# Performance work log

Hardware: AMD Instinct MI355X
Metric: run time of the kernel (lower is better)

The kernel has to match this reference:

```python
import jax, jax.numpy as jnp
import numpy as np

B, C, W, H = 8, 256, 64, 64
C8 = C // 8


def setup_inputs() -> dict:
    key = jax.random.key(0)
    ks = jax.random.split(key, 8)
    # xavier_uniform for 1x1 convs: bound = sqrt(6/(fan_in+fan_out))
    def xavier(k, out_c, in_c):
        bound = np.sqrt(6.0 / (in_c + out_c))
        return jax.random.uniform(k, (out_c, in_c), jnp.float32, -bound, bound)
    return {
        "x": jax.random.normal(ks[0], (B, C, W, H), jnp.float32),
        "Wf": xavier(ks[1], C8, C),
        "bf": jnp.zeros((C8,), jnp.float32),
        "Wg": xavier(ks[2], C8, C),
        "bg": jnp.zeros((C8,), jnp.float32),
        "Wh": xavier(ks[3], C, C),
        "bh": jnp.zeros((C,), jnp.float32),
        "gamma": jnp.zeros((1,), jnp.float32),
    }


def reference(x, Wf, bf, Wg, bg, Wh, bh, gamma):
    b, c, w, h = x.shape
    n = w * h
    xf = x.reshape(b, c, n)                                   # (B, C, N)
    # 1x1 convs == per-position channel GEMMs
    f = jnp.einsum('oc,bcn->bon', Wf, xf) + bf[None, :, None]  # (B, C/8, N)
    g = jnp.einsum('oc,bcn->bon', Wg, xf) + bg[None, :, None]  # (B, C/8, N)
    hh = jnp.einsum('oc,bcn->bon', Wh, xf) + bh[None, :, None] # (B, C, N)
    # attention[b,i,j] = softmax_j( f[b,:,i] . g[b,:,j] )
    att = jax.nn.softmax(jnp.einsum('boi,boj->bij', f, g), axis=-1)
    # torch.bmm(h, attention): out[b,c,i] = sum_k h[b,c,k] * att[b,k,i]
    sa = jnp.einsum('bck,bki->bci', hh, att).reshape(b, c, w, h)
    return gamma * sa + x
```

## Files before the change

kernel.cpp:

```cpp
#include <hip/hip_runtime.h>
#include <hip/hip_bf16.h>

#define BB 8
#define CC 256
#define NN 4096
#define LOG2E 1.44269504088896340736f
#define SHIFT 48.0f

typedef __attribute__((ext_vector_type(8))) short short8;
typedef __attribute__((ext_vector_type(4))) float f32x4;

static __device__ __forceinline__ unsigned short f2b(float x) {
  __hip_bfloat16 h = __float2bfloat16(x);
  return *reinterpret_cast<unsigned short*>(&h);
}
static __device__ __forceinline__ unsigned int pk2(float a, float b) {
  return (unsigned int)f2b(a) | ((unsigned int)f2b(b) << 16);
}


__global__ __launch_bounds__(256) void k_wprep(
    const float* __restrict__ Wf, const float* __restrict__ bfv,
    const float* __restrict__ Wg, const float* __restrict__ bgv,
    const float* __restrict__ Wh, const float* __restrict__ bhv,
    unsigned short* __restrict__ wA, float* __restrict__ ball)
{
  const int t = threadIdx.x;
  const int fi = blockIdx.x * 4 + (t >> 6);
  const int l = t & 63;
  const int mg = fi >> 3, kg = fi & 7;
  const int o = mg * 16 + (l & 15);
  const int c0 = kg * 32 + (l >> 4) * 8;
  const float* src; float scale = 1.0f;
  if (o < 32)      { src = Wf + (size_t)o * CC; scale = LOG2E; }
  else if (o < 64) { src = Wg + (size_t)(o - 32) * CC; }
  else             { src = Wh + (size_t)(o - 64) * CC; }
  float4 a = *(const float4*)(src + c0);
  float4 c = *(const float4*)(src + c0 + 4);
  short8 v;
  v[0] = (short)f2b(a.x * scale); v[1] = (short)f2b(a.y * scale);
  v[2] = (short)f2b(a.z * scale); v[3] = (short)f2b(a.w * scale);
  v[4] = (short)f2b(c.x * scale); v[5] = (short)f2b(c.y * scale);
  v[6] = (short)f2b(c.z * scale); v[7] = (short)f2b(c.w * scale);
  *(short8*)(wA + (size_t)fi * 512 + l * 8) = v;
  if (blockIdx.x == 0 && t < 320)
    ball[t] = (t < 32) ? bfv[t] * LOG2E : (t < 64) ? bgv[t - 32] : bhv[t - 64];
}

__global__ __launch_bounds__(512) void k_fgh(
    const float* __restrict__ x, const unsigned short* __restrict__ wA,
    const float* __restrict__ ball,
    unsigned short* __restrict__ fA, unsigned short* __restrict__ gB,
    unsigned short* __restrict__ hA)
{
  __shared__ __align__(16) char smem[41984];
  unsigned short* xb = (unsigned short*)smem;
  unsigned short* TL = (unsigned short*)smem;
  const int bid = blockIdx.x;
  const int b = bid & 7, i0 = (bid >> 3) * 64;
  const int t = threadIdx.x, w = t >> 6, l = t & 63;
  const int ig_w = w & 3, mg0 = (w >> 2) * 10;
  f32x4 acc[10] = {};
  for (int cc = 0; cc < 4; ++cc) {
    __syncthreads();
    {
      short8 v;
      const float* xp = x + ((size_t)b * CC + cc * 64 + w * 8) * NN + i0 + l;
      #pragma unroll
      for (int e = 0; e < 8; ++e) v[e] = (short)f2b(xp[(size_t)e * NN]);
      int frag = (w >> 2) * 4 + (l >> 4);
      int lp = (w & 3) * 16 + (l & 15);
      *(short8*)(xb + (frag * 64 + lp) * 8) = v;
    }
    __syncthreads();
    #pragma unroll
    for (int kg2 = 0; kg2 < 2; ++kg2) {
      short8 bfrag = *(const short8*)(xb + ((kg2 * 4 + ig_w) * 64 + l) * 8);
      int kg = cc * 2 + kg2;
      #pragma unroll
      for (int j = 0; j < 10; ++j) {
        short8 afrag = *(const short8*)(wA +
            ((size_t)((mg0 + j) * 8 + kg)) * 512 + l * 8);
        acc[j] = __builtin_amdgcn_mfma_f32_16x16x32_bf16(afrag, bfrag, acc[j], 0, 0, 0);
      }
    }
  }
  __syncthreads();
  #pragma unroll
  for (int j = 0; j < 10; ++j) {
    int ob = (mg0 + j) * 16 + (l >> 4) * 4;
    float4 bl = *(const float4*)(ball + ob);
    int irow = ig_w * 16 + (l & 15);
    ushort4 pv;
    pv.x = f2b(acc[j][0] + bl.x); pv.y = f2b(acc[j][1] + bl.y);
    pv.z = f2b(acc[j][2] + bl.z); pv.w = f2b(acc[j][3] + bl.w);
    *(ushort4*)(TL + irow * 328 + ob) = pv;
  }
  __syncthreads();
  if (t < 256) {
    int kg_p = t >> 6;
    int o8 = (l >> 4) * 8;
    int irow = kg_p * 16 + (l & 15);
    short8 vf = *(const short8*)(TL + irow * 328 + o8);
    short8 vg = *(const short8*)(TL + irow * 328 + 32 + o8);
    size_t kgG = (size_t)b * 256 + (i0 >> 4) + kg_p;
    *(short8*)(fA + kgG * 512 + l * 8) = vf;
    *(short8*)(gB + kgG * 512 + l * 8) = vg;
  }
  #pragma unroll
  for (int q = 0; q < 4; ++q) {
    int slot = t + q * 512;
    int fr = slot >> 6, ll = slot & 63;
    int cg = fr >> 1, kcl = fr & 1;
    int orow = 64 + cg * 16 + (ll & 15);
    int pbase = kcl * 32 + (ll >> 4) * 8;
    short8 v;
    #pragma unroll
    for (int e = 0; e < 8; ++e) v[e] = (short)TL[(pbase + e) * 328 + orow];
    size_t idx = (((size_t)b * 16 + cg) * 128 + (i0 >> 5) + kcl) * 512 + ll * 8;
    *(short8*)(hA + idx) = v;
  }
}

__global__ __launch_bounds__(512) void k_stats(
    const unsigned short* __restrict__ fA, const unsigned short* __restrict__ gB,
    float* __restrict__ cshift)
{
  __shared__ __align__(16) unsigned short sg[2][16 * 512];
  const int bid = blockIdx.x;
  const int b = bid & 7, kt = bid >> 3;
  const int t = threadIdx.x, w = t >> 6, l = t & 63;
  const int li = l & 15, lh = l >> 4;
  short8 af = *(const short8*)(fA + ((size_t)b * 256 + kt * 8 + w) * 512 + l * 8);
  const unsigned short* gb = gB + (size_t)b * 256 * 512;
  f32x4 zero = {0.f, 0.f, 0.f, 0.f};
  {
    uint4 v0 = *(const uint4*)(gb + ((size_t)(w * 2 + 0) * 64 + l) * 8);
    uint4 v1 = *(const uint4*)(gb + ((size_t)(w * 2 + 1) * 64 + l) * 8);
    *(uint4*)(&sg[0][((w * 2 + 0) * 64 + l) * 8]) = v0;
    *(uint4*)(&sg[0][((w * 2 + 1) * 64 + l) * 8]) = v1;
  }
  __syncthreads();
  float s[4] = {0.f, 0.f, 0.f, 0.f};
  for (int jt = 0; jt < 16; ++jt) {
    if (jt < 15) {
      uint4 v0 = *(const uint4*)(gb + ((size_t)((jt + 1) * 16 + w * 2 + 0) * 64 + l) * 8);
      uint4 v1 = *(const uint4*)(gb + ((size_t)((jt + 1) * 16 + w * 2 + 1) * 64 + l) * 8);
      unsigned short* dst = &sg[(jt + 1) & 1][0];
      *(uint4*)(dst + ((w * 2 + 0) * 64 + l) * 8) = v0;
      *(uint4*)(dst + ((w * 2 + 1) * 64 + l) * 8) = v1;
    }
    const unsigned short* src = &sg[jt & 1][0];
    #pragma unroll
    for (int jf = 0; jf < 16; ++jf) {
      short8 bfrag = *(const short8*)(src + (jf * 64 + l) * 8);
      f32x4 d = __builtin_amdgcn_mfma_f32_16x16x32_bf16(af, bfrag, zero, 0, 0, 0);
      s[0] += exp2f(d[0] - SHIFT);
      s[1] += exp2f(d[1] - SHIFT);
      s[2] += exp2f(d[2] - SHIFT);
      s[3] += exp2f(d[3] - SHIFT);
    }
    __syncthreads();
  }
  #pragma unroll
  for (int mk = 1; mk < 16; mk <<= 1)
    #pragma unroll
    for (int r = 0; r < 4; ++r) s[r] += __shfl_xor(s[r], mk);
  if (li == 0) {
    #pragma unroll
    for (int r = 0; r < 4; ++r) {
      size_t idx = (size_t)b * NN + (kt * 8 + w) * 16 + lh * 4 + r;
      cshift[idx] = SHIFT + log2f(fmaxf(s[r], 1e-30f));
    }
  }
}

__global__ __launch_bounds__(512, 4) void k_out(
    const unsigned short* __restrict__ fA, const unsigned short* __restrict__ gB,
    const unsigned short* __restrict__ hA,
    const float* __restrict__ csv,
    const float* __restrict__ x, const float* __restrict__ gamma,
    float* __restrict__ out)
{
  __shared__ __align__(16) unsigned short pbuf[2 * 16 * 512];
  const int bid = blockIdx.x;
  const int b = bid & 7, i0 = (bid >> 3) * 64;
  const int t = threadIdx.x, w = t >> 6, l = t & 63;
  const int li = l & 15, lh = l >> 4;
  const unsigned short* fAb = fA + ((size_t)b * 256 + w) * 512 + l * 8;
  const unsigned short* hAb = hA + ((size_t)b * 16 + w * 2) * (size_t)128 * 512 + l * 8;
  const float* cs = csv + (size_t)b * NN + w * 16 + lh * 4;
  short8 g[4];
  #pragma unroll
  for (int ig = 0; ig < 4; ++ig)
    g[ig] = *(const short8*)(gB + ((size_t)b * 256 + (i0 >> 4) + ig) * 512 + l * 8);
  const int pl = ((w & 1) * 2 + (lh >> 1)) * 16 + li;
  const int pwo = pl * 8 + (lh & 1) * 4;
  f32x4 zero = {0.f, 0.f, 0.f, 0.f};
  f32x4 acc[2][4] = {};
  short8 afc = *(const short8*)(fAb);
  float4 ccc = *(const float4*)(cs);
  #pragma unroll
  for (int ig = 0; ig < 4; ++ig) {
    f32x4 sfr = __builtin_amdgcn_mfma_f32_16x16x32_bf16(afc, g[ig], zero, 0, 0, 0);
    uint2 v;
    v.x = pk2(exp2f(sfr[0] - ccc.x), exp2f(sfr[1] - ccc.y));
    v.y = pk2(exp2f(sfr[2] - ccc.z), exp2f(sfr[3] - ccc.w));
    *(uint2*)(pbuf + ((size_t)((w >> 1) * 4 + ig)) * 512 + pwo) = v;
  }
  afc = *(const short8*)(fAb + (size_t)8 * 512);
  ccc = *(const float4*)(cs + 128);
  __syncthreads();
  for (int ch = 0; ch < 32; ++ch) {
    unsigned short* pb  = pbuf + (ch & 1) * (16 * 512);
    unsigned short* pnx = pbuf + ((ch + 1) & 1) * (16 * 512);
    short8 hf[8];
    #pragma unroll
    for (int cg = 0; cg < 2; ++cg)
      #pragma unroll
      for (int kb = 0; kb < 4; ++kb)
        hf[cg * 4 + kb] = *(const short8*)(hAb +
            ((size_t)cg * 128 + ch * 4 + kb) * 512);
    if (ch < 31) {
      #pragma unroll
      for (int ig = 0; ig < 4; ++ig) {
        f32x4 sfr = __builtin_amdgcn_mfma_f32_16x16x32_bf16(afc, g[ig], zero, 0, 0, 0);
        uint2 v;
        v.x = pk2(exp2f(sfr[0] - ccc.x), exp2f(sfr[1] - ccc.y));
        v.y = pk2(exp2f(sfr[2] - ccc.z), exp2f(sfr[3] - ccc.w));
        *(uint2*)(pnx + ((size_t)((w >> 1) * 4 + ig)) * 512 + pwo) = v;
      }
      const int ch2 = (ch < 30) ? (ch + 2) : 31;
      afc = *(const short8*)(fAb + (size_t)ch2 * 8 * 512);
      ccc = *(const float4*)(cs + ch2 * 128);
    }
    __builtin_amdgcn_s_setprio(1);
    #pragma unroll
    for (int kb = 0; kb < 4; ++kb)
      #pragma unroll
      for (int ig = 0; ig < 4; ++ig) {
        short8 pf = *(const short8*)(pb + ((kb * 4 + ig) * 64 + l) * 8);
        acc[0][ig] = __builtin_amdgcn_mfma_f32_16x16x32_bf16(pf, hf[kb], acc[0][ig], 0, 0, 0);
        acc[1][ig] = __builtin_amdgcn_mfma_f32_16x16x32_bf16(pf, hf[4 + kb], acc[1][ig], 0, 0, 0);
      }
    __builtin_amdgcn_s_setprio(0);
    __syncthreads();
  }
  const float gm = gamma[0];
  #pragma unroll
  for (int cg = 0; cg < 2; ++cg)
    #pragma unroll
    for (int ig = 0; ig < 4; ++ig) {
      int c = w * 32 + cg * 16 + li;
      int i = i0 + ig * 16 + lh * 4;
      size_t off = ((size_t)b * CC + c) * NN + i;
      float4 xv = *(const float4*)(x + off);
      float4 ov;
      ov.x = gm * acc[cg][ig][0] + xv.x;
      ov.y = gm * acc[cg][ig][1] + xv.y;
      ov.z = gm * acc[cg][ig][2] + xv.z;
      ov.w = gm * acc[cg][ig][3] + xv.w;
      *(float4*)(out + off) = ov;
    }
}

extern "C" void kernel_launch(void* const* d_in, const int* in_sizes, int n_in,
                              void* d_out, int out_size, void* d_ws, size_t ws_size,
                              hipStream_t stream)
{
  const float* x     = (const float*)d_in[0];
  const float* Wf    = (const float*)d_in[1];
  const float* bf    = (const float*)d_in[2];
  const float* Wg    = (const float*)d_in[3];
  const float* bg    = (const float*)d_in[4];
  const float* Wh    = (const float*)d_in[5];
  const float* bh    = (const float*)d_in[6];
  const float* gamma = (const float*)d_in[7];
  float* out = (float*)d_out;

  char* wsb = (char*)d_ws;
  float* cshift = (float*)(wsb + 131072);
  unsigned short* wA = (unsigned short*)(wsb + 262144);
  float* ball        = (float*)(wsb + 425984);
  unsigned short* fA = (unsigned short*)(wsb + 427520);
  unsigned short* gB = (unsigned short*)(wsb + 2524672);
  unsigned short* hA = (unsigned short*)(wsb + 4621824);

  k_wprep<<<40,  256, 0, stream>>>(Wf, bf, Wg, bg, Wh, bh, wA, ball);
  k_fgh  <<<512, 512, 0, stream>>>(x, wA, ball, fA, gB, hA);
  k_stats<<<256, 512, 0, stream>>>(fA, gB, cshift);
  k_out  <<<512, 512, 0, stream>>>(fA, gB, hA, cshift, x, gamma, out);
}
```

Measured before the change: 165.2 us.

## Split k_out key loop across two wave groups with LDS reduction

k_out now launches 1024 threads per block and splits the 32-chunk key dimension between two groups of 8 waves. Each group accumulates half of the output, and the partial sums are reduced through LDS before the residual write. The software-pipelined P precompute and the setprio hints are dropped in favour of a simpler compute-sync-MMA loop, on the bet that the extra waves hide latency. The costs are a larger LDS buffer, an extra reduction step, and a barrier on every chunk that serialises the exp and MMA phases.

After: 382.3 us. +131.4%, slower.

```diff
diff --git a/kernel.cpp b/kernel.cpp
--- a/kernel.cpp
+++ b/kernel.cpp
@@ -175,66 +175,52 @@
   }
 }
 
-__global__ __launch_bounds__(512, 4) void k_out(
+__global__ __launch_bounds__(1024, 8) void k_out(
     const unsigned short* __restrict__ fA, const unsigned short* __restrict__ gB,
     const unsigned short* __restrict__ hA,
     const float* __restrict__ csv,
     const float* __restrict__ x, const float* __restrict__ gamma,
     float* __restrict__ out)
 {
-  __shared__ __align__(16) unsigned short pbuf[2 * 16 * 512];
+  __shared__ __align__(16) unsigned short pbuf[4 * 16 * 512];
   const int bid = blockIdx.x;
   const int b = bid & 7, i0 = (bid >> 3) * 64;
   const int t = threadIdx.x, w = t >> 6, l = t & 63;
+  const int grp = w >> 3, wg = w & 7;
   const int li = l & 15, lh = l >> 4;
-  const unsigned short* fAb = fA + ((size_t)b * 256 + w) * 512 + l * 8;
-  const unsigned short* hAb = hA + ((size_t)b * 16 + w * 2) * (size_t)128 * 512 + l * 8;
-  const float* cs = csv + (size_t)b * NN + w * 16 + lh * 4;
-  short8 g[4];
+  const unsigned short* fAb = fA + ((size_t)b * 256 + wg) * 512 + l * 8;
+  const unsigned short* hAb = hA + ((size_t)b * 16 + wg * 2) * (size_t)128 * 512 + l * 8;
+  const float* cs = csv + (size_t)b * NN + wg * 16 + lh * 4;
+  short8 gfr[4];
   #pragma unroll
   for (int ig = 0; ig < 4; ++ig)
-    g[ig] = *(const short8*)(gB + ((size_t)b * 256 + (i0 >> 4) + ig) * 512 + l * 8);
-  const int pl = ((w & 1) * 2 + (lh >> 1)) * 16 + li;
+    gfr[ig] = *(const short8*)(gB + ((size_t)b * 256 + (i0 >> 4) + ig) * 512 + l * 8);
+  const int pl = ((wg & 1) * 2 + (lh >> 1)) * 16 + li;
   const int pwo = pl * 8 + (lh & 1) * 4;
+  unsigned short* pgrp = pbuf + grp * (2 * 16 * 512);
   f32x4 zero = {0.f, 0.f, 0.f, 0.f};
   f32x4 acc[2][4] = {};
-  short8 afc = *(const short8*)(fAb);
-  float4 ccc = *(const float4*)(cs);
-  #pragma unroll
-  for (int ig = 0; ig < 4; ++ig) {
-    f32x4 sfr = __builtin_amdgcn_mfma_f32_16x16x32_bf16(afc, g[ig], zero, 0, 0, 0);
-    uint2 v;
-    v.x = pk2(exp2f(sfr[0] - ccc.x), exp2f(sfr[1] - ccc.y));
-    v.y = pk2(exp2f(sfr[2] - ccc.z), exp2f(sfr[3] - ccc.w));
-    *(uint2*)(pbuf + ((size_t)((w >> 1) * 4 + ig)) * 512 + pwo) = v;
-  }
-  afc = *(const short8*)(fAb + (size_t)8 * 512);
-  ccc = *(const float4*)(cs + 128);
-  __syncthreads();
-  for (int ch = 0; ch < 32; ++ch) {
-    unsigned short* pb  = pbuf + (ch & 1) * (16 * 512);
-    unsigned short* pnx = pbuf + ((ch + 1) & 1) * (16 * 512);
+  for (int ch = 0; ch < 16; ++ch) {
+    const int ca = grp * 16 + ch;
     short8 hf[8];
     #pragma unroll
     for (int cg = 0; cg < 2; ++cg)
       #pragma unroll
       for (int kb = 0; kb < 4; ++kb)
         hf[cg * 4 + kb] = *(const short8*)(hAb +
-            ((size_t)cg * 128 + ch * 4 + kb) * 512);
-    if (ch < 31) {
-      #pragma unroll
-      for (int ig = 0; ig < 4; ++ig) {
-        f32x4 sfr = __builtin_amdgcn_mfma_f32_16x16x32_bf16(afc, g[ig], zero, 0, 0, 0);
-        uint2 v;
-        v.x = pk2(exp2f(sfr[0] - ccc.x), exp2f(sfr[1] - ccc.y));
-        v.y = pk2(exp2f(sfr[2] - ccc.z), exp2f(sfr[3] - ccc.w));
-        *(uint2*)(pnx + ((size_t)((w >> 1) * 4 + ig)) * 512 + pwo) = v;
-      }
-      const int ch2 = (ch < 30) ? (ch + 2) : 31;
-      afc = *(const short8*)(fAb + (size_t)ch2 * 8 * 512);
-      ccc = *(const float4*)(cs + ch2 * 128);
-    }
-    __builtin_amdgcn_s_setprio(1);
+            ((size_t)cg * 128 + ca * 4 + kb) * 512);
+    short8 af = *(const short8*)(fAb + (size_t)ca * 8 * 512);
+    float4 cc = *(const float4*)(cs + ca * 128);
+    unsigned short* pb = pgrp + (ch & 1) * (16 * 512);
+    #pragma unroll
+    for (int ig = 0; ig < 4; ++ig) {
+      f32x4 sfr = __builtin_amdgcn_mfma_f32_16x16x32_bf16(af, gfr[ig], zero, 0, 0, 0);
+      uint2 v;
+      v.x = pk2(exp2f(sfr[0] - cc.x), exp2f(sfr[1] - cc.y));
+      v.y = pk2(exp2f(sfr[2] - cc.z), exp2f(sfr[3] - cc.w));
+      *(uint2*)(pb + ((size_t)((wg >> 1) * 4 + ig)) * 512 + pwo) = v;
+    }
+    __syncthreads();
     #pragma unroll
     for (int kb = 0; kb < 4; ++kb)
       #pragma unroll
@@ -243,25 +229,37 @@
         acc[0][ig] = __builtin_amdgcn_mfma_f32_16x16x32_bf16(pf, hf[kb], acc[0][ig], 0, 0, 0);
         acc[1][ig] = __builtin_amdgcn_mfma_f32_16x16x32_bf16(pf, hf[4 + kb], acc[1][ig], 0, 0, 0);
       }
-    __builtin_amdgcn_s_setprio(0);
-    __syncthreads();
-  }
-  const float gm = gamma[0];
-  #pragma unroll
-  for (int cg = 0; cg < 2; ++cg)
-    #pragma unroll
-    for (int ig = 0; ig < 4; ++ig) {
-      int c = w * 32 + cg * 16 + li;
-      int i = i0 + ig * 16 + lh * 4;
-      size_t off = ((size_t)b * CC + c) * NN + i;
-      float4 xv = *(const float4*)(x + off);
-      float4 ov;
-      ov.x = gm * acc[cg][ig][0] + xv.x;
-      ov.y = gm * acc[cg][ig][1] + xv.y;
-      ov.z = gm * acc[cg][ig][2] + xv.z;
-      ov.w = gm * acc[cg][ig][3] + xv.w;
-      *(float4*)(out + off) = ov;
-    }
+  }
+  __syncthreads();
+  float* rbuf = (float*)pbuf;
+  if (grp == 1) {
+    #pragma unroll
+    for (int cg = 0; cg < 2; ++cg)
+      #pragma unroll
+      for (int ig = 0; ig < 4; ++ig)
+        *(f32x4*)(rbuf + ((size_t)((wg * 8 + cg * 4 + ig) * 64 + l)) * 4) = acc[cg][ig];
+  }
+  __syncthreads();
+  if (grp == 0) {
+    const float gm = gamma[0];
+    #pragma unroll
+    for (int cg = 0; cg < 2; ++cg)
+      #pragma unroll
+      for (int ig = 0; ig < 4; ++ig) {
+        f32x4 ob = *(const f32x4*)(rbuf + ((size_t)((wg * 8 + cg * 4 + ig) * 64 + l)) * 4);
+        f32x4 av = acc[cg][ig] + ob;
+        int c = wg * 32 + cg * 16 + li;
+        int i = i0 + ig * 16 + lh * 4;
+        size_t off = ((size_t)b * CC + c) * NN + i;
+        float4 xv = *(const float4*)(x + off);
+        float4 ov;
+        ov.x = gm * av[0] + xv.x;
+        ov.y = gm * av[1] + xv.y;
+        ov.z = gm * av[2] + xv.z;
+        ov.w = gm * av[3] + xv.w;
+        *(float4*)(out + off) = ov;
+      }
+  }
 }
 
 extern "C" void kernel_launch(void* const* d_in, const int* in_sizes, int n_in,
@@ -289,5 +287,5 @@
   k_wprep<<<40,  256, 0, stream>>>(Wf, bf, Wg, bg, Wh, bh, wA, ball);
   k_fgh  <<<512, 512, 0, stream>>>(x, wA, ball, fA, gB, hA);
   k_stats<<<256, 512, 0, stream>>>(fA, gB, cshift);
-  k_out  <<<512, 512, 0, stream>>>(fA, gB, hA, cshift, x, gamma, out);
-}
+  k_out  <<<512, 1024, 0, stream>>>(fA, gB, hA, cshift, x, gamma, out);
+}
```
